# Optimization experiments

Measured on AMD Instinct MI355X. Metric: run time of the kernel, lower is better.

Reference implementation:

```python
import jax, jax.numpy as jnp
import numpy as np

B, N, T, K = 2, 128, 1000, 30
L, S, R, DC = 4, 12, 8, 4  # layers, d_state, dt_rank, d_conv


def _ln(x, w, b, eps=1e-5):
    m = jnp.mean(x, -1, keepdims=True)
    v = jnp.var(x, -1, keepdims=True)
    return (x - m) * jax.lax.rsqrt(v + eps) * w + b


def setup_inputs():
    key = jax.random.key(0)
    ks = jax.random.split(key, 10)
    n = lambda k, shp, s=0.05: jax.random.normal(k, shp, jnp.float32) * s
    return {
        "x": jax.random.normal(ks[0], (B, N, T, K), jnp.float32),
        "ln_w": jnp.ones((L, N), jnp.float32),
        "ln_b": jnp.zeros((L, N), jnp.float32),
        "in_w": n(ks[1], (L, 2 * N, N)),
        "in_b": jnp.zeros((L, 2 * N), jnp.float32),
        "conv_w": n(ks[2], (L, N, DC), 0.3),
        "conv_b": jnp.zeros((L, N), jnp.float32),
        "xp_w": n(ks[3], (L, R + 2 * S, N)),
        "dtp_w": n(ks[4], (L, N, R)),
        "dtp_b": n(ks[5], (L, N), 0.5),
        "A_log": jnp.log(jnp.tile(jnp.arange(1.0, S + 1.0, dtype=jnp.float32), (L, N, 1))),
        "Dv": jnp.ones((L, N), jnp.float32),
        "out_w": n(ks[6], (L, N, N)),
        "out_b": jnp.zeros((L, N), jnp.float32),
        "cb_w": n(ks[7], (N, N), 0.09),
        "cb_b": jnp.zeros((N,), jnp.float32),
        "cb_ln_w": jnp.ones((N,), jnp.float32),
        "cb_ln_b": jnp.zeros((N,), jnp.float32),
        "fin_ln_w": jnp.ones((N,), jnp.float32),
        "fin_ln_b": jnp.zeros((N,), jnp.float32),
    }


def _mamba_block(seq, p):
    # seq: [BK, T, N]; canonical Mamba-1 block with pre-LN and residual
    lnw, lnb, iw, ib, cw, cb, xw, dw, db, alog, dv, ow, ob = p
    x = _ln(seq, lnw, lnb)
    xz = x @ iw.T + ib                         # [BK,T,2N]
    xc, z = jnp.split(xz, 2, axis=-1)
    # causal depthwise conv, kernel size DC
    xp = jnp.pad(xc, ((0, 0), (DC - 1, 0), (0, 0)))
    Tlen = xc.shape[1]
    conv = sum(xp[:, k:k + Tlen, :] * cw[:, k] for k in range(DC))
    xc = jax.nn.silu(conv + cb)
    dbc = xc @ xw.T                            # [BK,T,R+2S]
    dt = jax.nn.softplus(dbc[..., :R] @ dw.T + db)  # [BK,T,N]
    Bm = dbc[..., R:R + S]                     # [BK,T,S]
    Cm = dbc[..., R + S:]                      # [BK,T,S]
    A = -jnp.exp(alog)                         # [N,S]

    def step(h, inp):
        dt_t, B_t, C_t, x_t = inp              # [BK,N],[BK,S],[BK,S],[BK,N]
        dA = jnp.exp(dt_t[..., None] * A)      # [BK,N,S]
        h = dA * h + dt_t[..., None] * B_t[:, None, :] * x_t[..., None]
        y = jnp.einsum('bns,bs->bn', h, C_t)
        return h, y

    h0 = jnp.zeros((xc.shape[0], xc.shape[2], S), xc.dtype)
    xs = (jnp.swapaxes(dt, 0, 1), jnp.swapaxes(Bm, 0, 1),
          jnp.swapaxes(Cm, 0, 1), jnp.swapaxes(xc, 0, 1))
    _, ys = jax.lax.scan(step, h0, xs)
    y = jnp.swapaxes(ys, 0, 1) + dv * xc
    y = y * jax.nn.silu(z)
    return y @ ow.T + ob + seq


def reference(x, ln_w, ln_b, in_w, in_b, conv_w, conv_b, xp_w, dtp_w, dtp_b,
              A_log, Dv, out_w, out_b, cb_w, cb_b, cb_ln_w, cb_ln_b, fin_ln_w, fin_ln_b):
    b, n, t, k = x.shape
    seq = jnp.transpose(x, (0, 3, 2, 1)).reshape(b * k, t, n)  # [BK,T,N]

    def lstep(s, p):
        return _mamba_block(s, p), None

    seq, _ = jax.lax.scan(lstep, seq, (ln_w, ln_b, in_w, in_b, conv_w, conv_b,
                                       xp_w, dtp_w, dtp_b, A_log, Dv, out_w, out_b))
    main = jnp.transpose(seq.reshape(b, k, t, n), (0, 2, 1, 3))  # [B,T,K,N]
    cross = jax.nn.gelu(_ln(main @ cb_w.T + cb_b, cb_ln_w, cb_ln_b), approximate=False)
    feat = _ln(main + cross, fin_ln_w, fin_ln_b)
    return jnp.transpose(feat, (0, 3, 1, 2))  # [B,N,T,K]
```

## Files before the change

### kernel.cpp

```cpp
#include <hip/hip_runtime.h>
#include <math.h>

#define BKS 60
#define TL  1000
#define NF  128
#define SD  12
#define RD  8
#define NCH 32
#define CLEN 32
#define NTOK (BKS*TL)
#define MT  64
#define NBLK ((NTOK + MT - 1)/MT)
#define LNP 129
#define OFF_OW  131072
#define OFF_CBW 196608
#define OFF_XW  212992
#define WCNT    229376

typedef __bf16 bf16x8 __attribute__((ext_vector_type(8)));
typedef float  f32x4  __attribute__((ext_vector_type(4)));

__device__ __forceinline__ float siluf(float x){ return x / (1.f + __expf(-x)); }
__device__ __forceinline__ float softplusf(float x){
  if (x > 20.f) return x;
  float e = __expf(x);
  return (x < -20.f) ? e : __logf(1.f + e);
}
__device__ __forceinline__ ushort bf16r(float f){
  uint u = __float_as_uint(f);
  return (ushort)((u + 0x7FFFu + ((u>>16)&1u)) >> 16);
}
__device__ __forceinline__ float bf2f(ushort h){ return __uint_as_float(((uint)h)<<16); }

__global__ __launch_bounds__(256) void k_ingest(const float* __restrict__ x, float* __restrict__ seq){
  const int b = blockIdx.x / TL, t = blockIdx.x % TL;
  __shared__ float tile[30*NF];
  for (int e = threadIdx.x; e < 30*NF; e += 256){
    int n = e / 30, k = e - n*30;
    tile[k*NF + n] = x[((size_t)(b*NF + n)*TL + t)*30 + k];
  }
  __syncthreads();
  const size_t base = ((size_t)b*30)*TL*NF + (size_t)t*NF;
  for (int e = threadIdx.x; e < 30*NF; e += 256){
    int k = e >> 7, n = e & 127;
    seq[base + (size_t)k*TL*NF + n] = tile[e];
  }
}

__global__ __launch_bounds__(256) void k_wconv(
    const float* __restrict__ iw, const float* __restrict__ ow,
    const float* __restrict__ cw, const float* __restrict__ xw,
    ushort* __restrict__ wh, ushort* __restrict__ wl){
  const int idx = blockIdx.x*256 + threadIdx.x;
  if (idx >= WCNT) return;
  float v;
  if (idx < OFF_OW)       v = iw[idx];
  else if (idx < OFF_CBW) v = ow[idx - OFF_OW];
  else if (idx < OFF_XW)  v = cw[idx - OFF_CBW];
  else                    v = xw[idx - OFF_XW];
  const ushort h = bf16r(v);
  wh[idx] = h;
  wl[idx] = bf16r(v - bf2f(h));
}

__global__ __launch_bounds__(256) void k_ln_inproj(
    const float* __restrict__ seq, const float* __restrict__ lnw, const float* __restrict__ lnb,
    const ushort* __restrict__ wh, const ushort* __restrict__ wl, const float* __restrict__ ib,
    float* __restrict__ xcr, float* __restrict__ zb){
  __shared__ short xsh[MT*NF];
  __shared__ short xsl[MT*NF];
  const int tid = threadIdx.x;
  const int tok0 = blockIdx.x * MT;

  {
    const int j = tid >> 4, l16 = tid & 15;
    for (int it = 0; it < 4; ++it){
      const int t = j + 16*it;
      const int tok = tok0 + t;
      float v[8]; float s = 0.f, s2 = 0.f;
      if (tok < NTOK){
        const float* sp = seq + (size_t)tok*NF;
        #pragma unroll
        for (int i = 0; i < 8; ++i){ float f = sp[l16 + 16*i]; v[i] = f; s += f; s2 += f*f; }
      } else {
        #pragma unroll
        for (int i = 0; i < 8; ++i) v[i] = 0.f;
      }
      #pragma unroll
      for (int m = 1; m < 16; m <<= 1){ s += __shfl_xor(s, m, 64); s2 += __shfl_xor(s2, m, 64); }
      const float mean = s * (1.f/128.f);
      const float rstd = rsqrtf(s2*(1.f/128.f) - mean*mean + 1e-5f);
      const int swz = (t & 7) << 3;
      #pragma unroll
      for (int i = 0; i < 8; ++i){
        const int n = l16 + 16*i;
        const float f = (v[i]-mean)*rstd*lnw[n] + lnb[n];
        const ushort h = bf16r(f);
        xsh[t*NF + (n ^ swz)] = (short)h;
        xsl[t*NF + (n ^ swz)] = (short)bf16r(f - bf2f(h));
      }
    }
  }
  __syncthreads();

  const int w = tid >> 6, lane = tid & 63;
  const int cl = lane & 15, q8 = (lane >> 4) * 8;
  const int obase = w * 64;
  f32x4 acc[4][4];
  #pragma unroll
  for (int m = 0; m < 4; ++m)
    #pragma unroll
    for (int nt = 0; nt < 4; ++nt) acc[m][nt] = (f32x4){0.f,0.f,0.f,0.f};

  for (int c = 0; c < 4; ++c){
    bf16x8 ah[4], al[4];
    #pragma unroll
    for (int m = 0; m < 4; ++m){
      const int r = m*16 + cl;
      const int hi = r*NF + ((c*32 + q8) ^ ((r & 7) << 3));
      ah[m] = *(const bf16x8*)&xsh[hi];
      al[m] = *(const bf16x8*)&xsl[hi];
    }
    #pragma unroll
    for (int nt = 0; nt < 4; ++nt){
      const int o = obase + nt*16 + cl;
      const size_t wo = (size_t)o*NF + c*32 + q8;
      const bf16x8 bh = *(const bf16x8*)(wh + wo);
      const bf16x8 bl = *(const bf16x8*)(wl + wo);
      #pragma unroll
      for (int m = 0; m < 4; ++m){
        acc[m][nt] = __builtin_amdgcn_mfma_f32_16x16x32_bf16(ah[m], bh, acc[m][nt], 0, 0, 0);
        acc[m][nt] = __builtin_amdgcn_mfma_f32_16x16x32_bf16(al[m], bh, acc[m][nt], 0, 0, 0);
        acc[m][nt] = __builtin_amdgcn_mfma_f32_16x16x32_bf16(ah[m], bl, acc[m][nt], 0, 0, 0);
      }
    }
  }

  const int rbase = (lane >> 4) * 4;
  #pragma unroll
  for (int nt = 0; nt < 4; ++nt){
    const int o = obase + nt*16 + cl;
    const float bias = ib[o];
    float* dst = (o < NF) ? xcr : zb;
    const int oc = (o < NF) ? o : (o - NF);
    #pragma unroll
    for (int m = 0; m < 4; ++m)
      #pragma unroll
      for (int j2 = 0; j2 < 4; ++j2){
        const int tok = tok0 + m*16 + rbase + j2;
        if (tok < NTOK) dst[(size_t)tok*NF + oc] = acc[m][nt][j2] + bias;
      }
  }
}

__global__ __launch_bounds__(256) void k_conv_scan1(
    const float* __restrict__ xcr,
    const float* __restrict__ cw, const float* __restrict__ cb,
    const ushort* __restrict__ xwh, const ushort* __restrict__ xwl,
    const float* __restrict__ dw, const float* __restrict__ db,
    const float* __restrict__ alog,
    float* __restrict__ xcc, float* __restrict__ dcb,
    float* __restrict__ Bmb, float* __restrict__ Cmb,
    float* __restrict__ ap, float* __restrict__ hfb){
  __shared__ float smem[9600];
  float* sxr  = smem;
  float* sdt  = smem;
  short* xch  = (short*)(smem + 4480);
  short* xcl  = (short*)(smem + 6528);
  float* sdbc = smem + 8576;
  const int bid = blockIdx.x;
  const int sq = bid / NCH, cblk = bid - sq*NCH;
  const int t0 = cblk*CLEN;
  const int lim = (TL - t0 < CLEN) ? (TL - t0) : CLEN;
  const int tid = threadIdx.x;

  for (int i = 0; i < 5; ++i){
    const int e4 = tid + i*256;
    if (e4 < 35*32){
      const int r = e4 >> 5, n4 = (e4 & 31) << 2;
      const int t = t0 - 3 + r;
      float4 v = make_float4(0.f,0.f,0.f,0.f);
      if (t >= 0 && t < TL) v = *(const float4*)(xcr + ((size_t)sq*TL + t)*NF + n4);
      *(float4*)(sxr + r*NF + n4) = v;
    }
  }
  __syncthreads();

  #pragma unroll
  for (int i = 0; i < 4; ++i){
    const int e4 = tid + i*256;
    const int r = e4 >> 5, n4 = (e4 & 31) << 2;
    const float4 c0 = *(const float4*)(cw + (size_t)(n4+0)*4);
    const float4 c1 = *(const float4*)(cw + (size_t)(n4+1)*4);
    const float4 c2 = *(const float4*)(cw + (size_t)(n4+2)*4);
    const float4 c3 = *(const float4*)(cw + (size_t)(n4+3)*4);
    const float4 x0 = *(const float4*)(sxr + (r+0)*NF + n4);
    const float4 x1 = *(const float4*)(sxr + (r+1)*NF + n4);
    const float4 x2 = *(const float4*)(sxr + (r+2)*NF + n4);
    const float4 x3 = *(const float4*)(sxr + (r+3)*NF + n4);
    float4 a = *(const float4*)(cb + n4);
    a.x = fmaf(x3.x, c0.w, fmaf(x2.x, c0.z, fmaf(x1.x, c0.y, fmaf(x0.x, c0.x, a.x))));
    a.y = fmaf(x3.y, c1.w, fmaf(x2.y, c1.z, fmaf(x1.y, c1.y, fmaf(x0.y, c1.x, a.y))));
    a.z = fmaf(x3.z, c2.w, fmaf(x2.z, c2.z, fmaf(x1.z, c2.y, fmaf(x0.z, c2.x, a.z))));
    a.w = fmaf(x3.w, c3.w, fmaf(x2.w, c3.z, fmaf(x1.w, c3.y, fmaf(x0.w, c3.x, a.w))));
    a.x = siluf(a.x); a.y = siluf(a.y); a.z = siluf(a.z); a.w = siluf(a.w);
    const ushort h0 = bf16r(a.x), h1 = bf16r(a.y), h2 = bf16r(a.z), h3 = bf16r(a.w);
    const ushort l0 = bf16r(a.x - bf2f(h0)), l1 = bf16r(a.y - bf2f(h1));
    const ushort l2 = bf16r(a.z - bf2f(h2)), l3 = bf16r(a.w - bf2f(h3));
    const int bi = r*NF + (n4 ^ ((r & 7) << 3));
    *(uint2*)&xch[bi] = make_uint2((uint)h0 | ((uint)h1 << 16), (uint)h2 | ((uint)h3 << 16));
    *(uint2*)&xcl[bi] = make_uint2((uint)l0 | ((uint)l1 << 16), (uint)l2 | ((uint)l3 << 16));
    if (r < lim) *(float4*)(xcc + ((size_t)sq*TL + t0 + r)*NF + n4) = a;
  }
  __syncthreads();

  {
    const int w = tid >> 6, lane = tid & 63;
    const int cl = lane & 15, q8 = (lane >> 4) * 8;
    const int m = w & 1, nt = w >> 1;
    f32x4 acc = (f32x4){0.f,0.f,0.f,0.f};
    for (int c = 0; c < 4; ++c){
      const int r = m*16 + cl;
      const int ai = r*NF + ((c*32 + q8) ^ ((r & 7) << 3));
      const bf16x8 ah = *(const bf16x8*)&xch[ai];
      const bf16x8 al = *(const bf16x8*)&xcl[ai];
      const int o = nt*16 + cl;
      const size_t wo = (size_t)o*NF + c*32 + q8;
      const bf16x8 bh = *(const bf16x8*)(xwh + wo);
      const bf16x8 bl = *(const bf16x8*)(xwl + wo);
      acc = __builtin_amdgcn_mfma_f32_16x16x32_bf16(ah, bh, acc, 0, 0, 0);
      acc = __builtin_amdgcn_mfma_f32_16x16x32_bf16(al, bh, acc, 0, 0, 0);
      acc = __builtin_amdgcn_mfma_f32_16x16x32_bf16(ah, bl, acc, 0, 0, 0);
    }
    const int rb = m*16 + (lane >> 4)*4;
    const int o = nt*16 + cl;
    #pragma unroll
    for (int j = 0; j < 4; ++j)
      sdbc[(rb + j)*32 + o] = acc[j];
  }
  __syncthreads();

  #pragma unroll
  for (int i = 0; i < 16; ++i){
    const int e = tid + i*256;
    const int r = e >> 7, n = e & 127;
    const float4 b0 = *(const float4*)(sdbc + r*32);
    const float4 b1 = *(const float4*)(sdbc + r*32 + 4);
    const float4 w0 = *(const float4*)(dw + (size_t)n*8);
    const float4 w1 = *(const float4*)(dw + (size_t)n*8 + 4);
    float acc = db[n];
    acc = fmaf(b0.x, w0.x, acc); acc = fmaf(b0.y, w0.y, acc);
    acc = fmaf(b0.z, w0.z, acc); acc = fmaf(b0.w, w0.w, acc);
    acc = fmaf(b1.x, w1.x, acc); acc = fmaf(b1.y, w1.y, acc);
    acc = fmaf(b1.z, w1.z, acc); acc = fmaf(b1.w, w1.w, acc);
    sdt[e] = softplusf(acc);
  }
  if (tid < 64){
    const int t = tid >> 1, q = tid & 1;
    if (t < lim)
      *(float4*)(dcb + ((size_t)sq*TL + t0 + t)*8 + q*4) = *(const float4*)&sdbc[t*32 + q*4];
  }
  for (int e = tid; e < CLEN*2*SD; e += 256){
    int r = e / (2*SD), c = e - r*2*SD;
    if (r < lim){
      float v = sdbc[r*32 + 8 + c];
      size_t tok = (size_t)sq*TL + t0 + r;
      if (c < SD) Bmb[tok*SD + c] = v;
      else        Cmb[tok*SD + (c - SD)] = v;
    }
  }
  __syncthreads();

  {
    const int n = tid & 127, p = tid >> 7;
    float Av[6], h[6];
    #pragma unroll
    for (int s = 0; s < 6; ++s){
      Av[s] = -__expf(alog[(size_t)n*SD + p*6 + s]);
      h[s] = 0.f;
    }
    bool fast = true;
    #pragma unroll
    for (int s = 0; s < 6; ++s)
      fast = fast && (fabsf(Av[s] + (float)(p*6 + s + 1)) <= 1e-3f);
    float dts = 0.f;
    if (fast){
      for (int tt = 0; tt < lim; ++tt){
        const float dtv = sdt[tt*NF + n];
        const int xi = tt*NF + (n ^ ((tt & 7) << 3));
        const float xcv = bf2f((ushort)xch[xi]) + bf2f((ushort)xcl[xi]);
        float Bv[6];
        const float* br = sdbc + tt*32 + 8 + p*6;
        if (p == 0){
          const float4 a = *(const float4*)br;
          const float2 b = *(const float2*)(br + 4);
          Bv[0]=a.x; Bv[1]=a.y; Bv[2]=a.z; Bv[3]=a.w; Bv[4]=b.x; Bv[5]=b.y;
        } else {
          const float2 a = *(const float2*)br;
          const float4 b = *(const float4*)(br + 2);
          Bv[0]=a.x; Bv[1]=a.y; Bv[2]=b.x; Bv[3]=b.y; Bv[4]=b.z; Bv[5]=b.w;
        }
        const float dx = dtv * xcv;
        dts += dtv;
        const float q = __expf(-dtv);
        float dA;
        if (p == 0) dA = q;
        else { const float q2 = q*q; const float q4 = q2*q2; dA = q4*q2*q; }
        h[0] = fmaf(dA, h[0], dx*Bv[0]);
        #pragma unroll
        for (int s = 1; s < 6; ++s){ dA *= q; h[s] = fmaf(dA, h[s], dx*Bv[s]); }
      }
    } else {
      for (int tt = 0; tt < lim; ++tt){
        const float dtv = sdt[tt*NF + n];
        const int xi = tt*NF + (n ^ ((tt & 7) << 3));
        const float xcv = bf2f((ushort)xch[xi]) + bf2f((ushort)xcl[xi]);
        float Bv[6];
        const float* br = sdbc + tt*32 + 8 + p*6;
        if (p == 0){
          const float4 a = *(const float4*)br;
          const float2 b = *(const float2*)(br + 4);
          Bv[0]=a.x; Bv[1]=a.y; Bv[2]=a.z; Bv[3]=a.w; Bv[4]=b.x; Bv[5]=b.y;
        } else {
          const float2 a = *(const float2*)br;
          const float4 b = *(const float4*)(br + 2);
          Bv[0]=a.x; Bv[1]=a.y; Bv[2]=b.x; Bv[3]=b.y; Bv[4]=b.z; Bv[5]=b.w;
        }
        const float dx = dtv * xcv;
        dts += dtv;
        #pragma unroll
        for (int s = 0; s < 6; ++s){
          const float dA = __expf(dtv*Av[s]);
          h[s] = fmaf(dA, h[s], dx*Bv[s]);
        }
      }
    }
    const size_t base = (size_t)bid*SD*NF + n;
    #pragma unroll
    for (int s = 0; s < 6; ++s){
      ap [base + (p*6+s)*NF] = __expf(Av[s]*dts);
      hfb[base + (p*6+s)*NF] = h[s];
    }
  }
}

__global__ __launch_bounds__(128) void k_scan_combine(
    const float* __restrict__ ap, const float* __restrict__ hfb, float* __restrict__ hinit){
  const int sq = blockIdx.x;
  const int n = threadIdx.x;
  float h[SD];
  #pragma unroll
  for (int s = 0; s < SD; ++s) h[s] = 0.f;
  for (int c = 0; c < NCH; ++c){
    const size_t base = ((size_t)sq*NCH + c)*SD*NF + n;
    #pragma unroll
    for (int s = 0; s < SD; ++s){
      hinit[base + s*NF] = h[s];
      h[s] = fmaf(ap[base + s*NF], h[s], hfb[base + s*NF]);
    }
  }
}

__global__ __launch_bounds__(256) void k_back(
    const float* __restrict__ dcb, const float* __restrict__ xcc,
    const float* __restrict__ Bmb, const float* __restrict__ Cmb,
    const float* __restrict__ zb,
    const ushort* __restrict__ wh, const ushort* __restrict__ wl,
    const float* __restrict__ dw, const float* __restrict__ db,
    const float* __restrict__ alog, const float* __restrict__ hinit,
    const float* __restrict__ Dv, const float* __restrict__ ob,
    float* __restrict__ seq){
  __shared__ short xsh[MT*NF];
  __shared__ short xsl[MT*NF];
  const int bid = blockIdx.x;
  const int sq = bid >> 4, cb2 = bid & 15;
  const int t0 = cb2 * MT;
  const int lim = (TL - t0 < MT) ? (TL - t0) : MT;
  const int tid = threadIdx.x;

  {
    const int n = tid & 127, ch = tid >> 7;
    float Av[SD];
    {
      const float4 a0 = *(const float4*)(alog + (size_t)n*SD);
      const float4 a1 = *(const float4*)(alog + (size_t)n*SD + 4);
      const float4 a2 = *(const float4*)(alog + (size_t)n*SD + 8);
      const float t_[SD] = {a0.x,a0.y,a0.z,a0.w, a1.x,a1.y,a1.z,a1.w, a2.x,a2.y,a2.z,a2.w};
      #pragma unroll
      for (int s = 0; s < SD; ++s) Av[s] = -__expf(t_[s]);
    }
    bool fast = true;
    #pragma unroll
    for (int s = 0; s < SD; ++s)
      fast = fast && (fabsf(Av[s] + (float)(s + 1)) <= 1e-3f);
    const float4 dw0 = *(const float4*)(dw + (size_t)n*8);
    const float4 dw1 = *(const float4*)(dw + (size_t)n*8 + 4);
    const float dbn = db[n];
    const float dvn = Dv[n];
    float h[SD];
    {
      const size_t hb = ((size_t)(sq*NCH + cb2*2 + ch))*SD*NF + n;
      #pragma unroll
      for (int s = 0; s < SD; ++s) h[s] = hinit[hb + s*NF];
    }
    int steps = lim - ch*32; if (steps < 0) steps = 0; if (steps > 32) steps = 32;
    for (int tt = 0; tt < steps; ++tt){
      const int t = ch*32 + tt;
      const size_t gt = (size_t)sq*TL + t0 + t;
      const float4 d0 = *(const float4*)(dcb + gt*8);
      const float4 d1 = *(const float4*)(dcb + gt*8 + 4);
      float da = dbn;
      da = fmaf(d0.x,dw0.x, da); da = fmaf(d0.y,dw0.y, da);
      da = fmaf(d0.z,dw0.z, da); da = fmaf(d0.w,dw0.w, da);
      da = fmaf(d1.x,dw1.x, da); da = fmaf(d1.y,dw1.y, da);
      da = fmaf(d1.z,dw1.z, da); da = fmaf(d1.w,dw1.w, da);
      const float dtv = softplusf(da);
      const float xcv = xcc[gt*NF + n];
      const float zv  = zb [gt*NF + n];
      const float4 B0 = *(const float4*)(Bmb + gt*SD);
      const float4 B1 = *(const float4*)(Bmb + gt*SD + 4);
      const float4 B2 = *(const float4*)(Bmb + gt*SD + 8);
      const float4 C0 = *(const float4*)(Cmb + gt*SD);
      const float4 C1 = *(const float4*)(Cmb + gt*SD + 4);
      const float4 C2 = *(const float4*)(Cmb + gt*SD + 8);
      const float Bv[SD] = {B0.x,B0.y,B0.z,B0.w, B1.x,B1.y,B1.z,B1.w, B2.x,B2.y,B2.z,B2.w};
      const float Cv[SD] = {C0.x,C0.y,C0.z,C0.w, C1.x,C1.y,C1.z,C1.w, C2.x,C2.y,C2.z,C2.w};
      const float dx = dtv * xcv;
      float yv = 0.f;
      if (fast){
        const float q = __expf(-dtv);
        float dA = q;
        h[0] = fmaf(dA, h[0], dx*Bv[0]);
        yv = fmaf(h[0], Cv[0], yv);
        #pragma unroll
        for (int s = 1; s < SD; ++s){
          dA *= q;
          h[s] = fmaf(dA, h[s], dx*Bv[s]);
          yv = fmaf(h[s], Cv[s], yv);
        }
      } else {
        #pragma unroll
        for (int s = 0; s < SD; ++s){
          const float dA = __expf(dtv*Av[s]);
          h[s] = fmaf(dA, h[s], dx*Bv[s]);
          yv = fmaf(h[s], Cv[s], yv);
        }
      }
      const float yf = fmaf(dvn, xcv, yv) * siluf(zv);
      const ushort hh = bf16r(yf);
      const int bi = t*NF + (n ^ ((t & 7) << 3));
      xsh[bi] = (short)hh;
      xsl[bi] = (short)bf16r(yf - bf2f(hh));
    }
  }
  if (lim < MT){
    for (int e = tid; e < (MT - lim)*NF; e += 256){ xsh[lim*NF + e] = 0; xsl[lim*NF + e] = 0; }
  }
  __syncthreads();

  const int w = tid >> 6, lane = tid & 63;
  const int cl = lane & 15, q8 = (lane >> 4) * 8;
  const int obase = w * 32;
  f32x4 acc[4][2];
  #pragma unroll
  for (int m = 0; m < 4; ++m)
    #pragma unroll
    for (int nt = 0; nt < 2; ++nt) acc[m][nt] = (f32x4){0.f,0.f,0.f,0.f};

  for (int c = 0; c < 4; ++c){
    bf16x8 ah[4], al[4];
    #pragma unroll
    for (int m = 0; m < 4; ++m){
      const int r = m*16 + cl;
      const int hi = r*NF + ((c*32 + q8) ^ ((r & 7) << 3));
      ah[m] = *(const bf16x8*)&xsh[hi];
      al[m] = *(const bf16x8*)&xsl[hi];
    }
    #pragma unroll
    for (int nt = 0; nt < 2; ++nt){
      const int o = obase + nt*16 + cl;
      const size_t wo = (size_t)o*NF + c*32 + q8;
      const bf16x8 bh = *(const bf16x8*)(wh + wo);
      const bf16x8 bl = *(const bf16x8*)(wl + wo);
      #pragma unroll
      for (int m = 0; m < 4; ++m){
        acc[m][nt] = __builtin_amdgcn_mfma_f32_16x16x32_bf16(ah[m], bh, acc[m][nt], 0, 0, 0);
        acc[m][nt] = __builtin_amdgcn_mfma_f32_16x16x32_bf16(al[m], bh, acc[m][nt], 0, 0, 0);
        acc[m][nt] = __builtin_amdgcn_mfma_f32_16x16x32_bf16(ah[m], bl, acc[m][nt], 0, 0, 0);
      }
    }
  }

  const int rbase = (lane >> 4) * 4;
  #pragma unroll
  for (int nt = 0; nt < 2; ++nt){
    const int o = obase + nt*16 + cl;
    const float bias = ob[o];
    #pragma unroll
    for (int m = 0; m < 4; ++m)
      #pragma unroll
      for (int j2 = 0; j2 < 4; ++j2){
        const int lt = m*16 + rbase + j2;
        if (lt < lim){
          float* dst = seq + ((size_t)sq*TL + t0 + lt)*NF + o;
          *dst = *dst + acc[m][nt][j2] + bias;
        }
      }
  }
}

__global__ __launch_bounds__(256) void k_cross_gemm(
    const float* __restrict__ seq,
    const ushort* __restrict__ wh, const ushort* __restrict__ wl, const float* __restrict__ cbb,
    float* __restrict__ cross){
  __shared__ short xsh[MT*NF];
  __shared__ short xsl[MT*NF];
  const int tid = threadIdx.x;
  const int tok0 = blockIdx.x * MT;

  #pragma unroll
  for (int i = 0; i < 8; ++i){
    const int r  = (tid & 15) + ((i & 3) << 4);
    const int nq = (tid >> 4) + ((i >> 2) << 4);
    const int tok = tok0 + r;
    float4 v = make_float4(0.f,0.f,0.f,0.f);
    if (tok < NTOK){
      int b = tok / 30000, rr = tok - b*30000;
      int t = rr / 30, k = rr - t*30;
      v = *(const float4*)(seq + ((size_t)(b*30 + k)*TL + t)*NF + nq*4);
    }
    const ushort h0 = bf16r(v.x), h1 = bf16r(v.y), h2 = bf16r(v.z), h3 = bf16r(v.w);
    const ushort l0 = bf16r(v.x - bf2f(h0)), l1 = bf16r(v.y - bf2f(h1));
    const ushort l2 = bf16r(v.z - bf2f(h2)), l3 = bf16r(v.w - bf2f(h3));
    const int hi = r*NF + ((nq*4) ^ ((r & 7) << 3));
    *(uint2*)&xsh[hi] = make_uint2((uint)h0 | ((uint)h1 << 16), (uint)h2 | ((uint)h3 << 16));
    *(uint2*)&xsl[hi] = make_uint2((uint)l0 | ((uint)l1 << 16), (uint)l2 | ((uint)l3 << 16));
  }
  __syncthreads();

  const int w = tid >> 6, lane = tid & 63;
  const int cl = lane & 15, q8 = (lane >> 4) * 8;
  const int obase = w * 32;
  f32x4 acc[4][2];
  #pragma unroll
  for (int m = 0; m < 4; ++m)
    #pragma unroll
    for (int nt = 0; nt < 2; ++nt) acc[m][nt] = (f32x4){0.f,0.f,0.f,0.f};

  for (int c = 0; c < 4; ++c){
    bf16x8 ah[4], al[4];
    #pragma unroll
    for (int m = 0; m < 4; ++m){
      const int r = m*16 + cl;
      const int hi = r*NF + ((c*32 + q8) ^ ((r & 7) << 3));
      ah[m] = *(const bf16x8*)&xsh[hi];
      al[m] = *(const bf16x8*)&xsl[hi];
    }
    #pragma unroll
    for (int nt = 0; nt < 2; ++nt){
      const int o = obase + nt*16 + cl;
      const size_t wo = (size_t)o*NF + c*32 + q8;
      const bf16x8 bh = *(const bf16x8*)(wh + wo);
      const bf16x8 bl = *(const bf16x8*)(wl + wo);
      #pragma unroll
      for (int m = 0; m < 4; ++m){
        acc[m][nt] = __builtin_amdgcn_mfma_f32_16x16x32_bf16(ah[m], bh, acc[m][nt], 0, 0, 0);
        acc[m][nt] = __builtin_amdgcn_mfma_f32_16x16x32_bf16(al[m], bh, acc[m][nt], 0, 0, 0);
        acc[m][nt] = __builtin_amdgcn_mfma_f32_16x16x32_bf16(ah[m], bl, acc[m][nt], 0, 0, 0);
      }
    }
  }

  const int rbase = (lane >> 4) * 4;
  #pragma unroll
  for (int nt = 0; nt < 2; ++nt){
    const int o = obase + nt*16 + cl;
    const float bias = cbb[o];
    #pragma unroll
    for (int m = 0; m < 4; ++m)
      #pragma unroll
      for (int j2 = 0; j2 < 4; ++j2){
        const int tok = tok0 + m*16 + rbase + j2;
        if (tok < NTOK) cross[(size_t)tok*NF + o] = acc[m][nt][j2] + bias;
      }
  }
}

__global__ __launch_bounds__(256) void k_cross_ln(
    const float* __restrict__ seq, const float* __restrict__ cross,
    const float* __restrict__ clnw, const float* __restrict__ clnb,
    const float* __restrict__ flnw, const float* __restrict__ flnb,
    float* __restrict__ out){
  __shared__ float fs[32*LNP];
  const int tid = threadIdx.x;
  const int tok0 = blockIdx.x * 32;
  const int j16 = tid >> 4, l16 = tid & 15;

  for (int it = 0; it < 2; ++it){
    const int jj = j16 + 16*it;
    const int tok = tok0 + jj;
    const int b = tok / 30000, rr = tok - b*30000;
    const int t = rr / 30, k = rr - t*30;
    const float* cp = cross + (size_t)tok*NF;
    const float* mp = seq + ((size_t)(b*30 + k)*TL + t)*NF;
    float cv[8]; float s = 0.f, s2 = 0.f;
    #pragma unroll
    for (int i = 0; i < 8; ++i){
      float f = cp[l16 + 16*i]; cv[i] = f; s += f; s2 += f*f;
    }
    #pragma unroll
    for (int m = 1; m < 16; m <<= 1){ s += __shfl_xor(s, m, 64); s2 += __shfl_xor(s2, m, 64); }
    float mu = s * (1.f/128.f);
    float rs = rsqrtf(s2*(1.f/128.f) - mu*mu + 1e-5f);
    float rv[8]; float rsum = 0.f, rsum2 = 0.f;
    #pragma unroll
    for (int i = 0; i < 8; ++i){
      int n = l16 + 16*i;
      float cn = (cv[i] - mu)*rs*clnw[n] + clnb[n];
      float g = 0.5f*cn*(1.f + erff(cn*0.70710678118f));
      float res = mp[n] + g;
      rv[i] = res; rsum += res; rsum2 += res*res;
    }
    #pragma unroll
    for (int m = 1; m < 16; m <<= 1){ rsum += __shfl_xor(rsum, m, 64); rsum2 += __shfl_xor(rsum2, m, 64); }
    float mu2 = rsum * (1.f/128.f);
    float rs2 = rsqrtf(rsum2*(1.f/128.f) - mu2*mu2 + 1e-5f);
    #pragma unroll
    for (int i = 0; i < 8; ++i){
      int n = l16 + 16*i;
      fs[jj*LNP + n] = (rv[i] - mu2)*rs2*flnw[n] + flnb[n];
    }
  }
  __syncthreads();

  #pragma unroll
  for (int i = 0; i < 16; ++i){
    const int e = tid + i*256;
    const int j = e & 31, n = e >> 5;
    const int tok = tok0 + j;
    const int b = tok / 30000, rr = tok - b*30000;
    out[(size_t)(b*NF + n)*30000 + rr] = fs[j*LNP + n];
  }
}

extern "C" void kernel_launch(void* const* d_in, const int* in_sizes, int n_in,
                              void* d_out, int out_size, void* d_ws, size_t ws_size,
                              hipStream_t stream){
  const float* x       = (const float*)d_in[0];
  const float* ln_w    = (const float*)d_in[1];
  const float* ln_b    = (const float*)d_in[2];
  const float* in_w    = (const float*)d_in[3];
  const float* in_b    = (const float*)d_in[4];
  const float* conv_w  = (const float*)d_in[5];
  const float* conv_b  = (const float*)d_in[6];
  const float* xp_w    = (const float*)d_in[7];
  const float* dtp_w   = (const float*)d_in[8];
  const float* dtp_b   = (const float*)d_in[9];
  const float* A_log   = (const float*)d_in[10];
  const float* Dv      = (const float*)d_in[11];
  const float* out_w   = (const float*)d_in[12];
  const float* out_b   = (const float*)d_in[13];
  const float* cb_w    = (const float*)d_in[14];
  const float* cb_b    = (const float*)d_in[15];
  const float* cb_ln_w = (const float*)d_in[16];
  const float* cb_ln_b = (const float*)d_in[17];
  const float* fin_ln_w= (const float*)d_in[18];
  const float* fin_ln_b= (const float*)d_in[19];
  float* out = (float*)d_out;

  const size_t SEQSZ = (size_t)BKS*TL*NF;
  const size_t CHSZ  = (size_t)BKS*NF*NCH*SD;
  const size_t FBASE = 6*SEQSZ + 2*(size_t)BKS*TL*SD;
  const size_t BASE  = FBASE + WCNT;
  float* ws  = (float*)d_ws;
  float* seq = ws;
  float* xcr = ws + SEQSZ;
  float* zb  = ws + 2*SEQSZ;
  float* xcc = ws + 3*SEQSZ;
  float* dcb = ws + 4*SEQSZ;
  float* scr = ws + 5*SEQSZ;
  float* Bmb = ws + 6*SEQSZ;
  float* Cmb = Bmb + (size_t)BKS*TL*SD;
  ushort* wbh = (ushort*)(ws + FBASE);
  ushort* wbl = wbh + WCNT;
  if (ws_size < BASE*sizeof(float)) return;

  float* ap    = scr;
  float* hfb   = scr + CHSZ;
  float* hinit = xcr;
  float* cross = dcb;

  k_wconv<<<(WCNT + 255)/256, 256, 0, stream>>>(in_w, out_w, cb_w, xp_w, wbh, wbl);
  k_ingest<<<2*TL, 256, 0, stream>>>(x, seq);
  for (int l = 0; l < 4; ++l){
    k_ln_inproj<<<NBLK, 256, 0, stream>>>(seq, ln_w + l*NF, ln_b + l*NF,
        wbh + (size_t)l*32768, wbl + (size_t)l*32768, in_b + l*2*NF, xcr, zb);
    k_conv_scan1<<<BKS*NCH, 256, 0, stream>>>(xcr, conv_w + (size_t)l*NF*4, conv_b + l*NF,
        wbh + OFF_XW + (size_t)l*4096, wbl + OFF_XW + (size_t)l*4096,
        dtp_w + (size_t)l*NF*RD, dtp_b + l*NF,
        A_log + (size_t)l*NF*SD, xcc, dcb, Bmb, Cmb, ap, hfb);
    k_scan_combine<<<BKS, NF, 0, stream>>>(ap, hfb, hinit);
    k_back<<<BKS*16, 256, 0, stream>>>(dcb, xcc, Bmb, Cmb, zb,
        wbh + OFF_OW + (size_t)l*16384, wbl + OFF_OW + (size_t)l*16384,
        dtp_w + (size_t)l*NF*RD, dtp_b + l*NF,
        A_log + (size_t)l*NF*SD, hinit, Dv + l*NF, out_b + l*NF, seq);
  }
  k_cross_gemm<<<NBLK, 256, 0, stream>>>(seq, wbh + OFF_CBW, wbl + OFF_CBW, cb_b, cross);
  k_cross_ln<<<NTOK/32, 256, 0, stream>>>(seq, cross, cb_ln_w, cb_ln_b, fin_ln_w, fin_ln_b, out);
}
```

Baseline: 861.3 us.

## Store softplus dt from scan1 and vectorize LN loads/stores in in-proj

The first scan kernel now writes the full per-channel dt (after softplus) to global memory. The back kernel reads it directly instead of re-reading the 8-wide dt-rank vector and recomputing the projection and softplus on every step. The LN prologue of the in-proj kernel now uses float4 loads for the activations and LN weights, and packed uint4 stores of the bf16 hi/lo halves into shared memory. The trade is an extra 128-float-per-token write and read in place of 8 floats plus compute per step.

Result: faster. 777.1 us (-9.8%).

```diff
diff --git a/kernel.cpp b/kernel.cpp
--- a/kernel.cpp
+++ b/kernel.cpp
@@ -74,14 +74,24 @@
 
   {
     const int j = tid >> 4, l16 = tid & 15;
+    const float4 w0 = *(const float4*)(lnw + l16*8);
+    const float4 w1 = *(const float4*)(lnw + l16*8 + 4);
+    const float4 b0 = *(const float4*)(lnb + l16*8);
+    const float4 b1 = *(const float4*)(lnb + l16*8 + 4);
+    const float lw[8] = {w0.x,w0.y,w0.z,w0.w, w1.x,w1.y,w1.z,w1.w};
+    const float lb[8] = {b0.x,b0.y,b0.z,b0.w, b1.x,b1.y,b1.z,b1.w};
     for (int it = 0; it < 4; ++it){
       const int t = j + 16*it;
       const int tok = tok0 + t;
       float v[8]; float s = 0.f, s2 = 0.f;
       if (tok < NTOK){
-        const float* sp = seq + (size_t)tok*NF;
+        const float* sp = seq + (size_t)tok*NF + l16*8;
+        const float4 a0 = *(const float4*)sp;
+        const float4 a1 = *(const float4*)(sp + 4);
+        v[0]=a0.x; v[1]=a0.y; v[2]=a0.z; v[3]=a0.w;
+        v[4]=a1.x; v[5]=a1.y; v[6]=a1.z; v[7]=a1.w;
         #pragma unroll
-        for (int i = 0; i < 8; ++i){ float f = sp[l16 + 16*i]; v[i] = f; s += f; s2 += f*f; }
+        for (int i = 0; i < 8; ++i){ s += v[i]; s2 += v[i]*v[i]; }
       } else {
         #pragma unroll
         for (int i = 0; i < 8; ++i) v[i] = 0.f;
@@ -91,14 +101,22 @@
       const float mean = s * (1.f/128.f);
       const float rstd = rsqrtf(s2*(1.f/128.f) - mean*mean + 1e-5f);
       const int swz = (t & 7) << 3;
+      const int nb = (l16*8) ^ swz;
+      ushort hs[8], ls[8];
       #pragma unroll
       for (int i = 0; i < 8; ++i){
-        const int n = l16 + 16*i;
-        const float f = (v[i]-mean)*rstd*lnw[n] + lnb[n];
+        const float f = (v[i]-mean)*rstd*lw[i] + lb[i];
         const ushort h = bf16r(f);
-        xsh[t*NF + (n ^ swz)] = (short)h;
-        xsl[t*NF + (n ^ swz)] = (short)bf16r(f - bf2f(h));
-      }
+        hs[i] = h;
+        ls[i] = bf16r(f - bf2f(h));
+      }
+      uint4 hv, lv;
+      hv.x = (uint)hs[0] | ((uint)hs[1] << 16); hv.y = (uint)hs[2] | ((uint)hs[3] << 16);
+      hv.z = (uint)hs[4] | ((uint)hs[5] << 16); hv.w = (uint)hs[6] | ((uint)hs[7] << 16);
+      lv.x = (uint)ls[0] | ((uint)ls[1] << 16); lv.y = (uint)ls[2] | ((uint)ls[3] << 16);
+      lv.z = (uint)ls[4] | ((uint)ls[5] << 16); lv.w = (uint)ls[6] | ((uint)ls[7] << 16);
+      *(uint4*)&xsh[t*NF + nb] = hv;
+      *(uint4*)&xsl[t*NF + nb] = lv;
     }
   }
   __syncthreads();
@@ -159,7 +177,7 @@
     const ushort* __restrict__ xwh, const ushort* __restrict__ xwl,
     const float* __restrict__ dw, const float* __restrict__ db,
     const float* __restrict__ alog,
-    float* __restrict__ xcc, float* __restrict__ dcb,
+    float* __restrict__ xcc, float* __restrict__ dtb,
     float* __restrict__ Bmb, float* __restrict__ Cmb,
     float* __restrict__ ap, float* __restrict__ hfb){
   __shared__ float smem[9600];
@@ -253,12 +271,9 @@
     acc = fmaf(b0.z, w0.z, acc); acc = fmaf(b0.w, w0.w, acc);
     acc = fmaf(b1.x, w1.x, acc); acc = fmaf(b1.y, w1.y, acc);
     acc = fmaf(b1.z, w1.z, acc); acc = fmaf(b1.w, w1.w, acc);
-    sdt[e] = softplusf(acc);
-  }
-  if (tid < 64){
-    const int t = tid >> 1, q = tid & 1;
-    if (t < lim)
-      *(float4*)(dcb + ((size_t)sq*TL + t0 + t)*8 + q*4) = *(const float4*)&sdbc[t*32 + q*4];
+    const float dtv = softplusf(acc);
+    sdt[e] = dtv;
+    if (e < lim*NF) dtb[((size_t)sq*TL + t0)*NF + e] = dtv;
   }
   for (int e = tid; e < CLEN*2*SD; e += 256){
     int r = e / (2*SD), c = e - r*2*SD;
@@ -362,11 +377,10 @@
 }
 
 __global__ __launch_bounds__(256) void k_back(
-    const float* __restrict__ dcb, const float* __restrict__ xcc,
+    const float* __restrict__ dtb, const float* __restrict__ xcc,
     const float* __restrict__ Bmb, const float* __restrict__ Cmb,
     const float* __restrict__ zb,
     const ushort* __restrict__ wh, const ushort* __restrict__ wl,
-    const float* __restrict__ dw, const float* __restrict__ db,
     const float* __restrict__ alog, const float* __restrict__ hinit,
     const float* __restrict__ Dv, const float* __restrict__ ob,
     float* __restrict__ seq){
@@ -393,9 +407,6 @@
     #pragma unroll
     for (int s = 0; s < SD; ++s)
       fast = fast && (fabsf(Av[s] + (float)(s + 1)) <= 1e-3f);
-    const float4 dw0 = *(const float4*)(dw + (size_t)n*8);
-    const float4 dw1 = *(const float4*)(dw + (size_t)n*8 + 4);
-    const float dbn = db[n];
     const float dvn = Dv[n];
     float h[SD];
     {
@@ -407,14 +418,7 @@
     for (int tt = 0; tt < steps; ++tt){
       const int t = ch*32 + tt;
       const size_t gt = (size_t)sq*TL + t0 + t;
-      const float4 d0 = *(const float4*)(dcb + gt*8);
-      const float4 d1 = *(const float4*)(dcb + gt*8 + 4);
-      float da = dbn;
-      da = fmaf(d0.x,dw0.x, da); da = fmaf(d0.y,dw0.y, da);
-      da = fmaf(d0.z,dw0.z, da); da = fmaf(d0.w,dw0.w, da);
-      da = fmaf(d1.x,dw1.x, da); da = fmaf(d1.y,dw1.y, da);
-      da = fmaf(d1.z,dw1.z, da); da = fmaf(d1.w,dw1.w, da);
-      const float dtv = softplusf(da);
+      const float dtv = dtb[gt*NF + n];
       const float xcv = xcc[gt*NF + n];
       const float zv  = zb [gt*NF + n];
       const float4 B0 = *(const float4*)(Bmb + gt*SD);
@@ -677,7 +681,7 @@
   float* xcr = ws + SEQSZ;
   float* zb  = ws + 2*SEQSZ;
   float* xcc = ws + 3*SEQSZ;
-  float* dcb = ws + 4*SEQSZ;
+  float* dtb = ws + 4*SEQSZ;
   float* scr = ws + 5*SEQSZ;
   float* Bmb = ws + 6*SEQSZ;
   float* Cmb = Bmb + (size_t)BKS*TL*SD;
@@ -688,7 +692,7 @@
   float* ap    = scr;
   float* hfb   = scr + CHSZ;
   float* hinit = xcr;
-  float* cross = dcb;
+  float* cross = dtb;
 
   k_wconv<<<(WCNT + 255)/256, 256, 0, stream>>>(in_w, out_w, cb_w, xp_w, wbh, wbl);
   k_ingest<<<2*TL, 256, 0, stream>>>(x, seq);
@@ -698,11 +702,10 @@
     k_conv_scan1<<<BKS*NCH, 256, 0, stream>>>(xcr, conv_w + (size_t)l*NF*4, conv_b + l*NF,
         wbh + OFF_XW + (size_t)l*4096, wbl + OFF_XW + (size_t)l*4096,
         dtp_w + (size_t)l*NF*RD, dtp_b + l*NF,
-        A_log + (size_t)l*NF*SD, xcc, dcb, Bmb, Cmb, ap, hfb);
+        A_log + (size_t)l*NF*SD, xcc, dtb, Bmb, Cmb, ap, hfb);
     k_scan_combine<<<BKS, NF, 0, stream>>>(ap, hfb, hinit);
-    k_back<<<BKS*16, 256, 0, stream>>>(dcb, xcc, Bmb, Cmb, zb,
+    k_back<<<BKS*16, 256, 0, stream>>>(dtb, xcc, Bmb, Cmb, zb,
         wbh + OFF_OW + (size_t)l*16384, wbl + OFF_OW + (size_t)l*16384,
-        dtp_w + (size_t)l*NF*RD, dtp_b + l*NF,
         A_log + (size_t)l*NF*SD, hinit, Dv + l*NF, out_b + l*NF, seq);
   }
   k_cross_gemm<<<NBLK, 256, 0, stream>>>(seq, wbh + OFF_CBW, wbl + OFF_CBW, cb_b, cross);
```
